# Optimization experiments

Measured on AMD Instinct MI355X. Metric: run time of the kernel, lower is better.

## Reference

```python
import jax, jax.numpy as jnp
import numpy as np

MARGIN = 0.3
WARMUP_EPOCHS = 10
K = 5
ALPHA = 2.0
SAME_CAM_NEG_BOOST = 1.2
NEG_INF = jnp.float32(-jnp.inf)
POS_INF = jnp.float32(jnp.inf)


def setup_inputs() -> dict:
    key = jax.random.key(0)
    k1, k2, k3 = jax.random.split(key, 3)
    N, D = 8192, 2048
    feats = jax.random.normal(k1, (N, D), dtype=jnp.float32)
    labels = jax.random.randint(k2, (N,), 0, 256, dtype=jnp.int64)
    camids = jax.random.randint(k3, (N,), 0, 8, dtype=jnp.int64)
    return {"feats": feats, "labels": labels, "camids": camids, "epoch": 20}


def _topk_mean(dist_mat, mask, k, largest):
    # dist_mat [N,N], mask [N,N] bool. Per-row mean of k largest/smallest valid elems.
    if largest:
        work = jnp.where(mask, dist_mat, NEG_INF)
        vals, _ = jax.lax.top_k(work, k)            # [N,k] largest
        fallback = jnp.max(work, axis=1)
    else:
        work = jnp.where(mask, dist_mat, POS_INF)
        vals = -jax.lax.top_k(-work, k)[0]          # [N,k] smallest
        fallback = jnp.min(work, axis=1)
    is_valid = jnp.isfinite(vals)
    safe_sum = jnp.sum(jnp.where(is_valid, vals, 0.0), axis=1)
    counts = jnp.maximum(is_valid.sum(axis=1), 1)
    mean = safe_sum / counts
    return jnp.where(is_valid.any(axis=1), mean, fallback)


def _forward(feats, labels, camids, epoch):
    # (1) L2 normalize
    norm = jnp.linalg.norm(feats, axis=-1, keepdims=True)
    x = feats / jnp.maximum(norm, 1e-12)
    # Euclidean distance matrix [N,N]
    sq = jnp.sum(x * x, axis=1)
    dist2 = sq[:, None] + sq[None, :] - 2.0 * (x @ x.T)
    dist = jnp.sqrt(jnp.maximum(dist2, 1e-12))
    # masks (constants w.r.t. grad)
    N = feats.shape[0]
    eye = jnp.eye(N, dtype=bool)
    same_label = labels[:, None] == labels[None, :]
    same_cam = camids[:, None] == camids[None, :]
    is_pos = same_label & ~eye & ~same_cam   # cross_cam_pos=True
    is_neg = ~same_label & ~eye
    # boosted same-camera negatives
    neg_bias = jnp.where(is_neg & same_cam, SAME_CAM_NEG_BOOST, 1.0)
    dist_neg_sel = dist / jnp.maximum(neg_bias, 1e-6)
    # (2) top-k hard mining
    d_ap = _topk_mean(dist, is_pos, K, largest=True)
    d_an = _topk_mean(dist_neg_sel, is_neg, K, largest=False)
    # (5) hardness-aware weighting (no grad)
    w = jax.lax.stop_gradient(jax.nn.sigmoid(ALPHA * (d_ap - d_an)))
    w = w / jnp.maximum(w.mean(), 1e-12)
    # (3) margin schedule
    if epoch is not None and epoch < WARMUP_EPOCHS:
        per_sample = jax.nn.softplus(-(d_an - d_ap))
    else:
        per_sample = jax.nn.relu(d_ap - d_an + MARGIN)  # MarginRankingLoss, y=1
    loss = jnp.mean(w * per_sample)
    return loss, jax.lax.stop_gradient(d_ap), jax.lax.stop_gradient(d_an)


def reference(feats, labels, camids, epoch):
    return _forward(feats, labels, camids, epoch)
```

## Files before the change

### kernel.cpp

```cpp
#include <hip/hip_runtime.h>
#include <hip/hip_bf16.h>
#include <stdint.h>

typedef float   floatx4  __attribute__((ext_vector_type(4)));
typedef int     intx4    __attribute__((ext_vector_type(4)));
typedef int     intx8    __attribute__((ext_vector_type(8)));
typedef _Float16 halfx8  __attribute__((ext_vector_type(8)));
typedef _Float16 halfx4  __attribute__((ext_vector_type(4)));
typedef unsigned short ushort8 __attribute__((ext_vector_type(8)));

#define NROW 8192
#define NDIM 2048
#define BM 128
#define BKB 128
#define NSTRIP 64
#define NOFF (NSTRIP*(NSTRIP-1)/2)
#define NTILE (NSTRIP*(NSTRIP+1)/2)
#define DT_LD 136
#define KL_SYM 64
#define MERGE_BLOCKS 128

__device__ __forceinline__ void ins_desc(float (&a)[5], float v) {
#pragma unroll
    for (int k = 0; k < 5; ++k) { float hi = fmaxf(a[k], v); float lo = fminf(a[k], v); a[k] = hi; v = lo; }
}
__device__ __forceinline__ void ins_asc(float (&a)[5], float v) {
#pragma unroll
    for (int k = 0; k < 5; ++k) { float lo = fminf(a[k], v); float hi = fmaxf(a[k], v); a[k] = lo; v = hi; }
}

__device__ __forceinline__ void load_lds16(const void* g, void* l) {
    __builtin_amdgcn_global_load_lds((__attribute__((address_space(1))) void*)(void*)g,
                                     (__attribute__((address_space(3))) void*)l,
                                     16, 0, 0);
}

__global__ __launch_bounds__(256) void k_normalize(const float* __restrict__ feats,
                                                   unsigned char* __restrict__ xb,
                                                   float* __restrict__ sq) {
    const int row = blockIdx.x;
    const int t = threadIdx.x;
    const float* f = feats + (size_t)row * NDIM + t * 8;
    float4 v0 = *(const float4*)(f);
    float4 v1 = *(const float4*)(f + 4);
    float ss = v0.x*v0.x + v0.y*v0.y + v0.z*v0.z + v0.w*v0.w
             + v1.x*v1.x + v1.y*v1.y + v1.z*v1.z + v1.w*v1.w;
#pragma unroll
    for (int o = 32; o > 0; o >>= 1) ss += __shfl_down(ss, o);
    __shared__ float red[4];
    __shared__ float s_inv;
    if ((t & 63) == 0) red[t >> 6] = ss;
    __syncthreads();
    if (t == 0) {
        float tot = red[0] + red[1] + red[2] + red[3];
        float m = fmaxf(sqrtf(tot), 1e-12f);
        float inv = 1.0f / m;
        sq[row] = tot * inv * inv;
        s_inv = inv;
    }
    __syncthreads();
    float inv = s_inv;
    int w0 = __builtin_amdgcn_cvt_pk_fp8_f32(v0.x * inv, v0.y * inv, 0, false);
    w0     = __builtin_amdgcn_cvt_pk_fp8_f32(v0.z * inv, v0.w * inv, w0, true);
    int w1 = __builtin_amdgcn_cvt_pk_fp8_f32(v1.x * inv, v1.y * inv, 0, false);
    w1     = __builtin_amdgcn_cvt_pk_fp8_f32(v1.z * inv, v1.w * inv, w1, true);
    int2 pk; pk.x = w0; pk.y = w1;
    *(int2*)(xb + (size_t)row * NDIM + t * 8) = pk;
}

__device__ __forceinline__ void scan_half_row(const _Float16* Dt_,
        const unsigned short* labcam_cols,
        int srow, int shalf, int pli, float (&pos5)[5], float (&neg5)[5]) {
    const int jb = shalf * 64;
    const int sw = srow & 7;
#pragma unroll
    for (int c8 = 0; c8 < 8; ++c8) {
        halfx8 v = *(const halfx8*)(Dt_ + srow * DT_LD + ((shalf * 8 + (c8 ^ sw)) << 3));
        ushort8 lcv = *(const ushort8*)(labcam_cols + jb + c8 * 8);
#pragma unroll
        for (int e = 0; e < 8; ++e) {
            float d2 = (float)v[e];
            int x = pli ^ (int)lcv[e];
            bool same_label = (x & ~15) == 0;
            bool same_cam   = (x & 15) == 0;
            if (same_label) {
                if (!same_cam && d2 > pos5[4]) ins_desc(pos5, d2);
            } else {
                float vn = same_cam ? d2 * (1.0f / 1.44f) : d2;
                if (vn < neg5[4]) ins_asc(neg5, vn);
            }
        }
    }
}

__device__ __forceinline__ void emit_lists(float (&pos5)[5], float (&neg5)[5], int shalf,
        _Float16* posp, _Float16* negp, size_t gi, int slot) {
    float tp[5], tn[5];
#pragma unroll
    for (int k = 0; k < 5; ++k) { tp[k] = __shfl_xor(pos5[k], 1); tn[k] = __shfl_xor(neg5[k], 1); }
#pragma unroll
    for (int k = 0; k < 5; ++k) {
        if (tp[k] > pos5[4]) ins_desc(pos5, tp[k]);
        if (tn[k] < neg5[4]) ins_asc(neg5, tn[k]);
    }
    if (shalf == 0) {
        _Float16* pp = posp + (gi * KL_SYM + slot) * 5;
        _Float16* np = negp + (gi * KL_SYM + slot) * 5;
#pragma unroll
        for (int k = 0; k < 5; ++k) { pp[k] = (_Float16)pos5[k]; np[k] = (_Float16)neg5[k]; }
    }
}

__global__ __launch_bounds__(256, 3) void k_gemm_sym(
        const unsigned char* __restrict__ xb, const float* __restrict__ sq,
        const int* __restrict__ labels, const int* __restrict__ camids,
        _Float16* __restrict__ posp, _Float16* __restrict__ negp) {
    __shared__ __align__(16) char smem[BM * DT_LD * 2 + 4 * BM * 4];
    char* As = smem;
    char* Bs = smem + BM * BKB;
    _Float16* Dt = (_Float16*)smem;
    float* sqr_s = (float*)(smem + BM * DT_LD * 2);
    float* sqc_s = sqr_s + BM;
    unsigned short* labcam_a = (unsigned short*)(sqc_s + BM);
    unsigned short* labcam_b = labcam_a + BM;

    const int tid = threadIdx.x;
    const int w = tid >> 6, lane = tid & 63;
    const int wm = w >> 1, wn = w & 1;

    int a, b;
    {
        int bx = blockIdx.x;
        if (bx < NOFF) {
            a = (int)((1.0f + sqrtf(8.0f * (float)bx + 1.0f)) * 0.5f);
            while (a * (a - 1) / 2 > bx) --a;
            while (a * (a + 1) / 2 <= bx) ++a;
            b = bx - a * (a - 1) / 2;
        } else {
            a = b = bx - NOFF;
        }
    }
    const int r0 = a * BM, c0 = b * BM;

    if (tid < BM) {
        int gi = r0 + tid;
        sqr_s[tid] = sq[gi];
        labcam_a[tid] = (unsigned short)((labels[gi] << 4) | camids[gi]);
    } else {
        int t2 = tid - BM;
        int gj = c0 + t2;
        sqc_s[t2] = sq[gj];
        labcam_b[t2] = (unsigned short)((labels[gj] << 4) | camids[gj]);
    }
    __syncthreads();

    const int srow = tid >> 1;
    const int shalf = tid & 1;

    const int lr = lane >> 3;
    const int lc = ((lane & 7) ^ lr) * 16;
    const int m16 = lane & 15;
    const int quad = lane >> 4;
    const int s7 = m16 & 7;
    const int pc0 = ((2 * quad) ^ s7) * 16;
    const int pc1 = ((2 * quad + 1) ^ s7) * 16;

    floatx4 acc[4][4];
#pragma unroll
    for (int mi = 0; mi < 4; ++mi)
#pragma unroll
        for (int ni = 0; ni < 4; ++ni) {
            floatx4 z = {0.f, 0.f, 0.f, 0.f};
            acc[mi][ni] = z;
        }

    for (int kk = 0; kk < NDIM; kk += BKB) {
        __syncthreads();
#pragma unroll
        for (int q = 0; q < 4; ++q) {
            const int ra = w * 32 + q * 8;
            load_lds16(xb + (size_t)(r0 + ra + lr) * NDIM + kk + lc, As + ra * BKB);
            load_lds16(xb + (size_t)(c0 + ra + lr) * NDIM + kk + lc, Bs + ra * BKB);
        }
        __syncthreads();
        intx8 bfr[4];
#pragma unroll
        for (int ni = 0; ni < 4; ++ni) {
            const char* bp = Bs + (wn * 64 + ni * 16 + m16) * BKB;
            intx4 lo = *(const intx4*)(bp + pc0);
            intx4 hi = *(const intx4*)(bp + pc1);
            bfr[ni] = __builtin_shufflevector(lo, hi, 0, 1, 2, 3, 4, 5, 6, 7);
        }
#pragma unroll
        for (int mi = 0; mi < 4; ++mi) {
            const char* ap = As + (wm * 64 + mi * 16 + m16) * BKB;
            intx4 lo = *(const intx4*)(ap + pc0);
            intx4 hi = *(const intx4*)(ap + pc1);
            intx8 af = __builtin_shufflevector(lo, hi, 0, 1, 2, 3, 4, 5, 6, 7);
#pragma unroll
            for (int ni = 0; ni < 4; ++ni)
                acc[mi][ni] = __builtin_amdgcn_mfma_scale_f32_16x16x128_f8f6f4(
                    af, bfr[ni], acc[mi][ni], 0, 0, 0, 127, 0, 127);
        }
    }
    __syncthreads();

#pragma unroll
    for (int mi = 0; mi < 4; ++mi) {
        const int il = wm * 64 + mi * 16 + quad * 4;
#pragma unroll
        for (int ni = 0; ni < 4; ++ni) {
            const int jl = wn * 64 + ni * 16 + m16;
            const float sj = sqc_s[jl];
#pragma unroll
            for (int r = 0; r < 4; ++r) {
                float d2 = fmaxf(sqr_s[il + r] + sj - 2.0f * acc[mi][ni][r], 1e-12f);
                const int rw7 = (il + r) & 7;
                Dt[(il + r) * DT_LD + ((((jl >> 3) ^ rw7) << 3) | (jl & 7))] = (_Float16)d2;
            }
        }
    }
    __syncthreads();

    const float NINF = -__builtin_inff();
    const float PINF =  __builtin_inff();
    float pos5[5] = {NINF, NINF, NINF, NINF, NINF};
    float neg5[5] = {PINF, PINF, PINF, PINF, PINF};
    scan_half_row(Dt, labcam_b, srow, shalf, (int)labcam_a[srow], pos5, neg5);
    emit_lists(pos5, neg5, shalf, posp, negp, (size_t)(r0 + srow), b);

    if (a != b) {
        __syncthreads();
#pragma unroll
        for (int ni = 0; ni < 4; ++ni) {
            const int jl = wn * 64 + ni * 16 + m16;
            const float sj = sqc_s[jl];
            const int cw = jl & 7;
#pragma unroll
            for (int mi = 0; mi < 4; ++mi) {
                const int il = wm * 64 + mi * 16 + quad * 4;
                halfx4 h;
#pragma unroll
                for (int r = 0; r < 4; ++r)
                    h[r] = (_Float16)fmaxf(sqr_s[il + r] + sj - 2.0f * acc[mi][ni][r], 1e-12f);
                *(halfx4*)(Dt + jl * DT_LD + ((((il >> 3) ^ cw) << 3) | (il & 7))) = h;
            }
        }
        __syncthreads();
#pragma unroll
        for (int k = 0; k < 5; ++k) { pos5[k] = NINF; neg5[k] = PINF; }
        scan_half_row(Dt, labcam_a, srow, shalf, (int)labcam_b[srow], pos5, neg5);
        emit_lists(pos5, neg5, shalf, posp, negp, (size_t)(c0 + srow), a);
    }
}

__global__ __launch_bounds__(256) void k_merge_sym(const _Float16* __restrict__ posp,
        const _Float16* __restrict__ negp, const int* __restrict__ epoch_p,
        float* __restrict__ out, float* __restrict__ wsum_p, float* __restrict__ wpsum_p) {
    const int t = threadIdx.x;
    const int rq = t & 3;
    const int row = blockIdx.x * 64 + (t >> 2);
    const float NINF = -__builtin_inff(), PINF = __builtin_inff();
    float p5[5] = {NINF, NINF, NINF, NINF, NINF};
    float n5[5] = {PINF, PINF, PINF, PINF, PINF};
    const halfx8* pv8 = (const halfx8*)(posp + (size_t)row * (KL_SYM * 5) + rq * 80);
    const halfx8* nv8 = (const halfx8*)(negp + (size_t)row * (KL_SYM * 5) + rq * 80);
#pragma unroll
    for (int k = 0; k < 10; ++k) {
        halfx8 v = pv8[k];
#pragma unroll
        for (int e = 0; e < 8; ++e) { float f = (float)v[e]; if (f > p5[4]) ins_desc(p5, f); }
    }
#pragma unroll
    for (int k = 0; k < 10; ++k) {
        halfx8 v = nv8[k];
#pragma unroll
        for (int e = 0; e < 8; ++e) { float f = (float)v[e]; if (f < n5[4]) ins_asc(n5, f); }
    }
#pragma unroll
    for (int o = 1; o <= 2; o <<= 1) {
        float tp[5], tn[5];
#pragma unroll
        for (int k = 0; k < 5; ++k) { tp[k] = __shfl_xor(p5[k], o); tn[k] = __shfl_xor(n5[k], o); }
#pragma unroll
        for (int k = 0; k < 5; ++k) {
            if (tp[k] > p5[4]) ins_desc(p5, tp[k]);
            if (tn[k] < n5[4]) ins_asc(n5, tn[k]);
        }
    }
    float s = 0.f; int c = 0;
#pragma unroll
    for (int k = 0; k < 5; ++k) { bool fin = (p5[k] > NINF); s += fin ? sqrtf(p5[k]) : 0.f; c += fin ? 1 : 0; }
    float d_ap = (c > 0) ? s / (float)c : NINF;
    s = 0.f; c = 0;
#pragma unroll
    for (int k = 0; k < 5; ++k) { bool fin = (n5[k] < PINF); s += fin ? sqrtf(n5[k]) : 0.f; c += fin ? 1 : 0; }
    float d_an = (c > 0) ? s / (float)c : PINF;

    float w0 = 0.f, wp = 0.f;
    if (rq == 0) {
        out[1 + row] = d_ap;
        out[1 + NROW + row] = d_an;
        float diff = d_ap - d_an;
        w0 = 1.0f / (1.0f + expf(-2.0f * diff));
        float p;
        if (*epoch_p < 10) {
            p = fmaxf(diff, 0.0f) + log1pf(expf(-fabsf(diff)));
        } else {
            p = fmaxf(diff + 0.3f, 0.0f);
        }
        wp = w0 * p;
    }
#pragma unroll
    for (int o = 32; o > 0; o >>= 1) { w0 += __shfl_down(w0, o); wp += __shfl_down(wp, o); }
    __shared__ float rw[4], rp[4];
    if ((t & 63) == 0) { rw[t >> 6] = w0; rp[t >> 6] = wp; }
    __syncthreads();
    if (t == 0) {
        wsum_p[blockIdx.x]  = rw[0] + rw[1] + rw[2] + rw[3];
        wpsum_p[blockIdx.x] = rp[0] + rp[1] + rp[2] + rp[3];
    }
}

__global__ void k_finalize(const float* __restrict__ wsum_p, const float* __restrict__ wpsum_p,
                           float* __restrict__ out) {
    if (threadIdx.x == 0) {
        float sw = 0.f, swp = 0.f;
        for (int i = 0; i < MERGE_BLOCKS; ++i) { sw += wsum_p[i]; swp += wpsum_p[i]; }
        float M = fmaxf(sw / (float)NROW, 1e-12f);
        out[0] = swp / ((float)NROW * M);
    }
}

extern "C" void kernel_launch(void* const* d_in, const int* in_sizes, int n_in,
                              void* d_out, int out_size, void* d_ws, size_t ws_size,
                              hipStream_t stream) {
    const float* feats  = (const float*)d_in[0];
    const int*   labels = (const int*)d_in[1];
    const int*   camids = (const int*)d_in[2];
    const int*   epoch  = (const int*)d_in[3];
    float* out = (float*)d_out;
    char* ws = (char*)d_ws;

    unsigned char* xb = (unsigned char*)ws;
    float* sq = (float*)(ws + 16777216);
    const size_t HALF_LIST_BYTES = (size_t)NROW * KL_SYM * 5 * 2;
    _Float16* posp = (_Float16*)(ws + 16777216 + 32768);
    _Float16* negp = (_Float16*)(ws + 16777216 + 32768 + HALF_LIST_BYTES);
    float* wsum_p  = (float*)(ws + 16777216 + 32768 + 2 * HALF_LIST_BYTES);
    float* wpsum_p = wsum_p + MERGE_BLOCKS;

    k_normalize<<<NROW, 256, 0, stream>>>(feats, xb, sq);
    k_gemm_sym<<<NTILE, 256, 0, stream>>>(xb, sq, labels, camids, posp, negp);
    k_merge_sym<<<MERGE_BLOCKS, 256, 0, stream>>>(posp, negp, epoch, out, wsum_p, wpsum_p);
    k_finalize<<<1, 64, 0, stream>>>(wsum_p, wpsum_p, out);
}
```

Baseline: 250.7 us.

## Vectorize top-5 scan with packed half2 branchless masks and rotate LDS swizzle

Rewrites the per-row top-5 hard-mining scan so each lane handles two fp16 distances at once. It uses packed half2 min/max sorting networks and bitmask selects in place of per-element float compares and branches, then merges the two halves with an alignbit swap. The distance-tile LDS layout changes from an XOR swizzle to an additive rotation so whole 16-byte chunks can be loaded as int vectors. k_finalize now reduces the partial sums with a wavefront shuffle instead of a serial loop on one thread. The negative-branch insertion is now unconditional, and the boost scaling is done in fp16, which may cost a little precision.

```diff
diff --git a/kernel.cpp b/kernel.cpp
--- a/kernel.cpp
+++ b/kernel.cpp
@@ -7,6 +7,8 @@
 typedef int     intx8    __attribute__((ext_vector_type(8)));
 typedef _Float16 halfx8  __attribute__((ext_vector_type(8)));
 typedef _Float16 halfx4  __attribute__((ext_vector_type(4)));
+typedef _Float16 half2v  __attribute__((ext_vector_type(2)));
+typedef short   short2v  __attribute__((ext_vector_type(2)));
 typedef unsigned short ushort8 __attribute__((ext_vector_type(8)));
 
 #define NROW 8192
@@ -29,6 +31,39 @@
     for (int k = 0; k < 5; ++k) { float lo = fminf(a[k], v); float hi = fmaxf(a[k], v); a[k] = lo; v = hi; }
 }
 
+__device__ __forceinline__ int   h2bits(half2v v) { return __builtin_bit_cast(int, v); }
+__device__ __forceinline__ half2v bits2h(int v)   { return __builtin_bit_cast(half2v, v); }
+__device__ __forceinline__ int bfi(int m, int a, int b) { return (m & a) | (~m & b); }
+__device__ __forceinline__ int nzmask16(int v) {
+    short2v s = __builtin_bit_cast(short2v, v);
+    short2v n = (short2v)(0) - s;
+    int o = v | __builtin_bit_cast(int, n);
+    short2v m = __builtin_bit_cast(short2v, o) >> 15;
+    return __builtin_bit_cast(int, m);
+}
+__device__ __forceinline__ int nzmask16_small(int v) {
+    short2v s = __builtin_bit_cast(short2v, v);
+    short2v n = (short2v)(0) - s;
+    short2v m = n >> 15;
+    return __builtin_bit_cast(int, m);
+}
+__device__ __forceinline__ void ins_desc2(half2v (&a)[5], half2v v) {
+#pragma unroll
+    for (int k = 0; k < 5; ++k) {
+        half2v hi = __builtin_elementwise_max(a[k], v);
+        half2v lo = __builtin_elementwise_min(a[k], v);
+        a[k] = hi; v = lo;
+    }
+}
+__device__ __forceinline__ void ins_asc2(half2v (&a)[5], half2v v) {
+#pragma unroll
+    for (int k = 0; k < 5; ++k) {
+        half2v lo = __builtin_elementwise_min(a[k], v);
+        half2v hi = __builtin_elementwise_max(a[k], v);
+        a[k] = lo; v = hi;
+    }
+}
+
 __device__ __forceinline__ void load_lds16(const void* g, void* l) {
     __builtin_amdgcn_global_load_lds((__attribute__((address_space(1))) void*)(void*)g,
                                      (__attribute__((address_space(3))) void*)l,
@@ -72,25 +107,46 @@
         const unsigned short* labcam_cols,
         int srow, int shalf, int pli, float (&pos5)[5], float (&neg5)[5]) {
     const int jb = shalf * 64;
-    const int sw = srow & 7;
+    const int s2 = 2 * (srow & 7);
+    const int pli2 = pli * 0x00010001;
+    const int ONE2  = 0x3C003C00;
+    const int BOOST2= 0x398E398E;
+    const int PINF2 = 0x7C007C00;
+    const int NINF2 = 0xFC00FC00;
+    half2v p5[5], n5[5];
+#pragma unroll
+    for (int k = 0; k < 5; ++k) { p5[k] = bits2h(NINF2); n5[k] = bits2h(PINF2); }
 #pragma unroll
     for (int c8 = 0; c8 < 8; ++c8) {
-        halfx8 v = *(const halfx8*)(Dt_ + srow * DT_LD + ((shalf * 8 + (c8 ^ sw)) << 3));
-        ushort8 lcv = *(const ushort8*)(labcam_cols + jb + c8 * 8);
-#pragma unroll
-        for (int e = 0; e < 8; ++e) {
-            float d2 = (float)v[e];
-            int x = pli ^ (int)lcv[e];
-            bool same_label = (x & ~15) == 0;
-            bool same_cam   = (x & 15) == 0;
-            if (same_label) {
-                if (!same_cam && d2 > pos5[4]) ins_desc(pos5, d2);
-            } else {
-                float vn = same_cam ? d2 * (1.0f / 1.44f) : d2;
-                if (vn < neg5[4]) ins_asc(neg5, vn);
-            }
-        }
-    }
+        const int pc = ((shalf * 8 + c8) + s2) & 15;
+        intx4 v  = *(const intx4*)(Dt_ + srow * DT_LD + pc * 8);
+        intx4 lc = *(const intx4*)(labcam_cols + jb + c8 * 8);
+#pragma unroll
+        for (int e = 0; e < 4; ++e) {
+            const int d2p = v[e];
+            const int x   = pli2 ^ lc[e];
+            const int mdl = nzmask16(x & 0xFFF0FFF0);
+            const int mdc = nzmask16_small(x & 0x000F000F);
+            const int mul = bfi(mdc, ONE2, BOOST2);
+            half2v nv = bits2h(d2p) * bits2h(mul);
+            nv = bits2h(bfi(mdl, h2bits(nv), PINF2));
+            ins_asc2(n5, nv);
+            const int pmask = mdc & ~mdl;
+            half2v pv = bits2h(bfi(pmask, d2p, NINF2));
+            half2v chk = __builtin_elementwise_max(pv, p5[4]);
+            if (h2bits(chk) != h2bits(p5[4])) ins_desc2(p5, pv);
+        }
+    }
+    half2v tp[5], tn[5];
+#pragma unroll
+    for (int k = 0; k < 5; ++k) {
+        tp[k] = bits2h((int)__builtin_amdgcn_alignbit((unsigned)h2bits(p5[k]), (unsigned)h2bits(p5[k]), 16));
+        tn[k] = bits2h((int)__builtin_amdgcn_alignbit((unsigned)h2bits(n5[k]), (unsigned)h2bits(n5[k]), 16));
+    }
+#pragma unroll
+    for (int k = 0; k < 5; ++k) { ins_desc2(p5, tp[k]); ins_asc2(n5, tn[k]); }
+#pragma unroll
+    for (int k = 0; k < 5; ++k) { pos5[k] = (float)p5[k][0]; neg5[k] = (float)n5[k][0]; }
 }
 
 __device__ __forceinline__ void emit_lists(float (&pos5)[5], float (&neg5)[5], int shalf,
@@ -215,17 +271,14 @@
 #pragma unroll
             for (int r = 0; r < 4; ++r) {
                 float d2 = fmaxf(sqr_s[il + r] + sj - 2.0f * acc[mi][ni][r], 1e-12f);
-                const int rw7 = (il + r) & 7;
-                Dt[(il + r) * DT_LD + ((((jl >> 3) ^ rw7) << 3) | (jl & 7))] = (_Float16)d2;
+                const int pch = (((jl >> 3) + 2 * ((il + r) & 7)) & 15);
+                Dt[(il + r) * DT_LD + (pch << 3) + (jl & 7)] = (_Float16)d2;
             }
         }
     }
     __syncthreads();
 
-    const float NINF = -__builtin_inff();
-    const float PINF =  __builtin_inff();
-    float pos5[5] = {NINF, NINF, NINF, NINF, NINF};
-    float neg5[5] = {PINF, PINF, PINF, PINF, PINF};
+    float pos5[5], neg5[5];
     scan_half_row(Dt, labcam_b, srow, shalf, (int)labcam_a[srow], pos5, neg5);
     emit_lists(pos5, neg5, shalf, posp, negp, (size_t)(r0 + srow), b);
 
@@ -235,7 +288,7 @@
         for (int ni = 0; ni < 4; ++ni) {
             const int jl = wn * 64 + ni * 16 + m16;
             const float sj = sqc_s[jl];
-            const int cw = jl & 7;
+            const int cw2 = 2 * (jl & 7);
 #pragma unroll
             for (int mi = 0; mi < 4; ++mi) {
                 const int il = wm * 64 + mi * 16 + quad * 4;
@@ -243,12 +296,11 @@
 #pragma unroll
                 for (int r = 0; r < 4; ++r)
                     h[r] = (_Float16)fmaxf(sqr_s[il + r] + sj - 2.0f * acc[mi][ni][r], 1e-12f);
-                *(halfx4*)(Dt + jl * DT_LD + ((((il >> 3) ^ cw) << 3) | (il & 7))) = h;
+                const int pch = (((il >> 3) + cw2) & 15);
+                *(halfx4*)(Dt + jl * DT_LD + (pch << 3) + (il & 7)) = h;
             }
         }
         __syncthreads();
-#pragma unroll
-        for (int k = 0; k < 5; ++k) { pos5[k] = NINF; neg5[k] = PINF; }
         scan_half_row(Dt, labcam_a, srow, shalf, (int)labcam_b[srow], pos5, neg5);
         emit_lists(pos5, neg5, shalf, posp, negp, (size_t)(c0 + srow), a);
     }
@@ -324,9 +376,12 @@
 
 __global__ void k_finalize(const float* __restrict__ wsum_p, const float* __restrict__ wpsum_p,
                            float* __restrict__ out) {
-    if (threadIdx.x == 0) {
-        float sw = 0.f, swp = 0.f;
-        for (int i = 0; i < MERGE_BLOCKS; ++i) { sw += wsum_p[i]; swp += wpsum_p[i]; }
+    const int t = threadIdx.x;
+    float sw  = wsum_p[t]  + wsum_p[t + 64];
+    float swp = wpsum_p[t] + wpsum_p[t + 64];
+#pragma unroll
+    for (int o = 32; o > 0; o >>= 1) { sw += __shfl_down(sw, o); swp += __shfl_down(swp, o); }
+    if (t == 0) {
         float M = fmaxf(sw / (float)NROW, 1e-12f);
         out[0] = swp / ((float)NROW * M);
     }
```

Measured after the change: 243.8 us. 2.7% less time.
